# Performance work log

Measured on AMD Instinct MI355X. Metric: run time of the kernel, lower is better.

The kernel has to match this reference:

```python
import jax, jax.numpy as jnp
import numpy as np

H = 1.0  # primo_h
N_GRID = 768


def _grid_mesh(n):
    ii, jj = np.meshgrid(np.arange(n - 1), np.arange(n - 1), indexing='ij')
    v00 = (ii * n + jj).ravel(); v10 = ((ii + 1) * n + jj).ravel()
    v01 = (ii * n + jj + 1).ravel(); v11 = ((ii + 1) * n + jj + 1).ravel()
    tri1 = np.stack([v00, v10, v01], 1); tri2 = np.stack([v10, v11, v01], 1)
    return np.concatenate([tri1, tri2], 0).astype(np.int32)  # [F,3]


def _face_adjacency(faces):
    # faces: [F,3] -> edges [E,2] (sorted vertex pairs), face_ids [E,2]
    F = faces.shape[0]
    fe = np.stack([faces[:, [0, 1]], faces[:, [1, 2]], faces[:, [2, 0]]], 1).reshape(-1, 2)
    fe = np.sort(fe, axis=1)
    fid = np.repeat(np.arange(F, dtype=np.int32), 3)
    order = np.lexsort((fe[:, 1], fe[:, 0]))
    fs, fi = fe[order], fid[order]
    same = np.all(fs[:-1] == fs[1:], axis=1)
    k = np.nonzero(same)[0]
    edges = fs[k].astype(np.int32)
    face_ids = np.stack([fi[k], fi[k + 1]], 1).astype(np.int32)
    return edges, face_ids


def setup_inputs() -> dict:
    key = jax.random.key(0)
    k1, k2, k3 = jax.random.split(key, 3)
    faces_np = _grid_mesh(N_GRID)                      # [F,3]
    edges_np, face_ids_np = _face_adjacency(faces_np)  # [E,2],[E,2]
    F = faces_np.shape[0]
    V = N_GRID * N_GRID
    return {
        'transformed_prism': jax.random.normal(k1, (F, 3, 3), dtype=jnp.float32),
        'rotations': jax.random.normal(k2, (F, 3, 3), dtype=jnp.float32),
        'verts': jax.random.normal(k3, (1, V, 3), dtype=jnp.float32),
        'faces': jnp.asarray(faces_np.T),       # [3,F], matches torch forward arg
        'edges': jnp.asarray(edges_np),
        'face_ids': jnp.asarray(face_ids_np),
    }


def _verts_id_face(Ft, E, Q):
    # Ft: [F,3] faces; E: [e,2] edge vertex ids; Q: [e,2] adjacent face ids
    fa, fb = Ft[Q[:, 0]], Ft[Q[:, 1]]  # [e,3]

    def find(fv, tgt):
        return jnp.where(fv[:, 0] == tgt, 0,
               jnp.where(fv[:, 1] == tgt, 1,
               jnp.where(fv[:, 2] == tgt, 2, -1)))

    return jnp.stack([find(fa, E[:, 0]), find(fa, E[:, 1]),
                      find(fb, E[:, 0]), find(fb, E[:, 1])], axis=1)  # [e,4]


def reference(transformed_prism, rotations, verts, faces, edges, face_ids):
    tp = transformed_prism
    bs = verts.shape[0]
    v = verts.reshape(-1, 3)
    Ft = faces.T  # [F,3]

    # per-face normals (vectorized version of the original per-face loop)
    e1 = tp[:, 0] - tp[:, 1]
    e2 = tp[:, 0] - tp[:, 2]
    nrm = jnp.cross(e1, e2)
    normals = nrm / jnp.linalg.norm(nrm, axis=-1, keepdims=True)  # [F,3]

    # face areas
    p1, p2, p3 = v[Ft[:, 0]], v[Ft[:, 1]], v[Ft[:, 2]]
    face_areas = 0.5 * jnp.linalg.norm(jnp.cross(p2 - p1, p3 - p1), axis=1)

    # faithful to original: normals indexed by edge VERTEX ids
    n1, n2 = normals[edges[:, 0]], normals[edges[:, 1]]
    fid1, fid2 = face_ids[:, 0], face_ids[:, 1]
    r1, r2 = rotations[fid1], rotations[fid2]

    ftv = _verts_id_face(Ft, edges, face_ids)  # [e,4]
    v1_p1, v2_p1 = tp[fid1, ftv[:, 0]], tp[fid1, ftv[:, 1]]
    v1_p2, v2_p2 = tp[fid2, ftv[:, 2]], tp[fid2, ftv[:, 3]]

    p1n1 = jnp.einsum('ec,ecd->ed', n1, r1)
    p1n2 = jnp.einsum('ec,ecd->ed', n2, r1)
    p2n1 = jnp.einsum('ec,ecd->ed', n1, r2)
    p2n2 = jnp.einsum('ec,ecd->ed', n2, r2)

    A = jnp.stack([v1_p1 + p1n1 * H, v2_p1 + p1n2 * H,
                   v1_p1 - p1n1 * H, v2_p1 - p1n2 * H], axis=1)  # [e,4,3]
    B = jnp.stack([v1_p2 + p2n1 * H, v2_p2 + p2n2 * H,
                   v1_p2 - p2n1 * H, v2_p2 - p2n2 * H], axis=1)
    D = A - B

    # coeff[p,q] = 2^{-|i_p-i_q|-|j_p-j_q|}, (i,j) over {0,1}^2
    idx = jnp.array([[0, 0], [0, 1], [1, 0], [1, 1]], dtype=jnp.float32)
    coeff = 2.0 ** (-jnp.abs(idx[:, None] - idx[None, :]).sum(-1))  # [4,4]
    pair = jnp.einsum('epc,eqc->epq', D, D)
    energy = (pair * coeff).sum((1, 2)) / 9.0  # [e]

    weight = jnp.sum((v[edges[:, 0]] - v[edges[:, 1]]) ** 2, axis=1) \
             / (face_areas[fid1] + face_areas[fid2])
    return (energy * weight).sum() / bs
```

## Files before the change

### kernel.cpp

```cpp
#include <hip/hip_runtime.h>


struct __attribute__((aligned(4))) F4s { float a, b, c, d; };
struct F3 { float x, y, z; };
struct R9 { float v[9]; };
struct R6 { float v[6]; };

__device__ __forceinline__ R9 load9(const float* __restrict__ p) {
    R9 r;
    F4s u0 = *(const F4s*)p;
    F4s u1 = *(const F4s*)(p + 4);
    r.v[0] = u0.a; r.v[1] = u0.b; r.v[2] = u0.c; r.v[3] = u0.d;
    r.v[4] = u1.a; r.v[5] = u1.b; r.v[6] = u1.c; r.v[7] = u1.d;
    r.v[8] = p[8];
    return r;
}

__device__ __forceinline__ R6 load6(const float* __restrict__ p) {
    R6 r;
    F4s u = *(const F4s*)p;
    r.v[0] = u.a; r.v[1] = u.b; r.v[2] = u.c; r.v[3] = u.d;
    r.v[4] = p[4]; r.v[5] = p[5];
    return r;
}

__device__ __forceinline__ F3 load3(const float* __restrict__ p) {
    F3 r; r.x = p[0]; r.y = p[1]; r.z = p[2]; return r;
}

__device__ __forceinline__ F3 normal_of(const R9& r) {
    float e1x = r.v[0] - r.v[3], e1y = r.v[1] - r.v[4], e1z = r.v[2] - r.v[5];
    float e2x = r.v[0] - r.v[6], e2y = r.v[1] - r.v[7], e2z = r.v[2] - r.v[8];
    float nx = e1y * e2z - e1z * e2y;
    float ny = e1z * e2x - e1x * e2z;
    float nz = e1x * e2y - e1y * e2x;
    float inv = 1.0f / sqrtf(nx * nx + ny * ny + nz * nz);
    F3 o; o.x = nx * inv; o.y = ny * inv; o.z = nz * inv; return o;
}

__device__ __forceinline__ float tri_area(const F3& p, const F3& q, const F3& r) {
    float ax = q.x - p.x, ay = q.y - p.y, az = q.z - p.z;
    float bx = r.x - p.x, by = r.y - p.y, bz = r.z - p.z;
    float cx = ay * bz - az * by, cy = az * bx - ax * bz, cz = ax * by - ay * bx;
    return 0.5f * sqrtf(cx * cx + cy * cy + cz * cz);
}

__device__ __forceinline__ float edge_ew(const float* u1, const float* u2,
                                         const float* w1, const float* w2,
                                         const float* rA, const float* rB,
                                         const F3& n1, const F3& n2,
                                         const F3& pa, const F3& pb,
                                         float asum) {
    float ux = u1[0] - u2[0], uy = u1[1] - u2[1], uz = u1[2] - u2[2];
    float wx = w1[0] - w2[0], wy = w1[1] - w2[1], wz = w1[2] - w2[2];

    float d0 = rA[0] - rB[0], d1 = rA[1] - rB[1], d2 = rA[2] - rB[2];
    float d3 = rA[3] - rB[3], d4 = rA[4] - rB[4], d5 = rA[5] - rB[5];
    float d6 = rA[6] - rB[6], d7 = rA[7] - rB[7], d8 = rA[8] - rB[8];

    float ax = n1.x * d0 + n1.y * d3 + n1.z * d6;
    float ay = n1.x * d1 + n1.y * d4 + n1.z * d7;
    float az = n1.x * d2 + n1.y * d5 + n1.z * d8;
    float bx = n2.x * d0 + n2.y * d3 + n2.z * d6;
    float by = n2.x * d1 + n2.y * d4 + n2.z * d7;
    float bz = n2.x * d2 + n2.y * d5 + n2.z * d8;

    float uu = ux * ux + uy * uy + uz * uz;
    float ww = wx * wx + wy * wy + wz * wz;
    float uw = ux * wx + uy * wy + uz * wz;
    float aa = ax * ax + ay * ay + az * az;
    float bb = bx * bx + by * by + bz * bz;
    float ab = ax * bx + ay * by + az * bz;
    float energy = (3.0f * (uu + ww + uw) + (aa + bb + ab)) * (1.0f / 9.0f);

    float dx = pa.x - pb.x, dy = pa.y - pb.y, dz = pa.z - pb.z;
    return energy * (dx * dx + dy * dy + dz * dz) / asum;
}

__global__ __launch_bounds__(256) void fused_kernel(
        const float* __restrict__ tp,
        const float* __restrict__ rot,
        const float* __restrict__ verts,
        double* __restrict__ partials,
        int n) {
    const int m = n - 1;
    const int Q = m * m;
    const int tid = threadIdx.x;
    int q = blockIdx.x * 256 + tid;
    bool valid = q < Q;
    int qc = valid ? q : Q - 1;
    int i = qc / m;
    int j = qc - i * m;

    int v00 = i * n + j;
    R9 tA = load9(tp + (size_t)9 * v00);
    R9 tB = load9(tp + (size_t)9 * (v00 + 1));
    R9 tC = load9(tp + (size_t)9 * (v00 + n));
    F3 p00 = load3(verts + (size_t)3 * v00);
    F3 p01 = load3(verts + (size_t)3 * (v00 + 1));
    F3 p10 = load3(verts + (size_t)3 * (v00 + n));
    F3 p11 = load3(verts + (size_t)3 * (v00 + n + 1));
    int iu = (i > 0) ? (i - 1) : 0;
    int jl = (j > 0) ? (j - 1) : 0;
    F3 pup = load3(verts + (size_t)3 * ((size_t)iu * n + (j + 1)));
    F3 plf = load3(verts + (size_t)3 * ((size_t)(i + 1) * n + jl));

    int f1  = i * m + j;
    int f2c = Q + f1;
    int f2u = Q + iu * m + j;
    int f2l = Q + i * m + jl;
    R9 t1 = load9(tp  + (size_t)9 * f1);
    R9 t2 = load9(tp  + (size_t)9 * f2c);
    R9 r1 = load9(rot + (size_t)9 * f1);
    R9 r2 = load9(rot + (size_t)9 * f2c);
    R6 th = load6(tp  + (size_t)9 * f2u);
    R9 rh = load9(rot + (size_t)9 * f2u);
    R6 tv = load6(tp  + (size_t)9 * f2l + 3);
    R9 rv = load9(rot + (size_t)9 * f2l);

    F3 nA = normal_of(tA);
    F3 nB = normal_of(tB);
    F3 nC = normal_of(tC);
    float a1    = tri_area(p00, p10, p01);
    float a2c   = tri_area(p10, p11, p01);
    float a2up  = tri_area(p00, p01, pup);
    float a2lf  = tri_area(plf, p10, p00);

    float sum = edge_ew(t1.v + 6, t2.v + 6, t1.v + 3, t2.v + 0, r1.v, r2.v,
                        nB, nC, p01, p10, a1 + a2c);
    float eh = edge_ew(t1.v + 0, th.v + 0, t1.v + 6, th.v + 3, r1.v, rh.v,
                       nA, nB, p00, p01, a1 + a2up);
    float ev = edge_ew(t1.v + 0, tv.v + 3, t1.v + 3, tv.v + 0, r1.v, rv.v,
                       nA, nC, p00, p10, a1 + a2lf);
    sum += (i > 0 ? eh : 0.0f);
    sum += (j > 0 ? ev : 0.0f);

    double term = valid ? (double)sum : 0.0;

#pragma unroll
    for (int off = 32; off > 0; off >>= 1) term += __shfl_down(term, off, 64);
    __shared__ double sred[4];
    int lane = tid & 63, wid = tid >> 6;
    if (lane == 0) sred[wid] = term;
    __syncthreads();
    if (tid == 0)
        partials[blockIdx.x] = sred[0] + sred[1] + sred[2] + sred[3];
}

__global__ __launch_bounds__(256) void finalize_kernel(
        const double* __restrict__ partials, int P, float* __restrict__ out) {
    double s = 0.0;
    for (int i = threadIdx.x; i < P; i += 256) s += partials[i];
#pragma unroll
    for (int off = 32; off > 0; off >>= 1) s += __shfl_down(s, off, 64);
    __shared__ double sred[4];
    int lane = threadIdx.x & 63, wid = threadIdx.x >> 6;
    if (lane == 0) sred[wid] = s;
    __syncthreads();
    if (threadIdx.x == 0) out[0] = (float)(sred[0] + sred[1] + sred[2] + sred[3]);
}

extern "C" void kernel_launch(void* const* d_in, const int* in_sizes, int n_in,
                              void* d_out, int out_size, void* d_ws, size_t ws_size,
                              hipStream_t stream) {
    const float* tp    = (const float*)d_in[0];
    const float* rot   = (const float*)d_in[1];
    const float* verts = (const float*)d_in[2];

    int V = in_sizes[2] / 3;
    int n = (int)(sqrtf((float)V) + 0.5f);
    int m = n - 1;
    int Q = m * m;

    double* partials = (double*)d_ws;
    float*  out      = (float*)d_out;

    int P = (Q + 255) / 256;
    fused_kernel<<<P, 256, 0, stream>>>(tp, rot, verts, partials, n);
    finalize_kernel<<<1, 256, 0, stream>>>(partials, P, out);
}
```

Before: 155.6 us.

## Tile faces, normals and verts into shared memory with halo reuse

Switches to a 2D block tiling (4 rows x 64 cols) where second-triangle prism/rotation data, per-vertex normals and vertex positions for the tile plus halo are staged in LDS. Neighbouring threads then read shared neighbours from LDS instead of issuing redundant global gathers, and each normal is computed once rather than three times. This costs a block-wide sync, about 50KB of LDS per block that limits occupancy, and halo overhead.

```diff
diff --git a/kernel.cpp b/kernel.cpp
--- a/kernel.cpp
+++ b/kernel.cpp
@@ -1,10 +1,18 @@
 #include <hip/hip_runtime.h>
 
+
+#define BI 4
+#define BJ 64
+#define FR (BI + 1)
+#define FC (BJ + 1)
+#define NR (BI + 1)
+#define NC (BJ + 1)
+#define VR (BI + 2)
+#define VC (BJ + 2)
 
 struct __attribute__((aligned(4))) F4s { float a, b, c, d; };
 struct F3 { float x, y, z; };
 struct R9 { float v[9]; };
-struct R6 { float v[6]; };
 
 __device__ __forceinline__ R9 load9(const float* __restrict__ p) {
     R9 r;
@@ -16,16 +24,8 @@
     return r;
 }
 
-__device__ __forceinline__ R6 load6(const float* __restrict__ p) {
-    R6 r;
-    F4s u = *(const F4s*)p;
-    r.v[0] = u.a; r.v[1] = u.b; r.v[2] = u.c; r.v[3] = u.d;
-    r.v[4] = p[4]; r.v[5] = p[5];
-    return r;
-}
-
-__device__ __forceinline__ F3 load3(const float* __restrict__ p) {
-    F3 r; r.x = p[0]; r.y = p[1]; r.z = p[2]; return r;
+__device__ __forceinline__ int iclamp(int x, int lo, int hi) {
+    return x < lo ? lo : (x > hi ? hi : x);
 }
 
 __device__ __forceinline__ F3 normal_of(const R9& r) {
@@ -38,9 +38,10 @@
     F3 o; o.x = nx * inv; o.y = ny * inv; o.z = nz * inv; return o;
 }
 
-__device__ __forceinline__ float tri_area(const F3& p, const F3& q, const F3& r) {
-    float ax = q.x - p.x, ay = q.y - p.y, az = q.z - p.z;
-    float bx = r.x - p.x, by = r.y - p.y, bz = r.z - p.z;
+__device__ __forceinline__ float tri_area_p(const float* p, const float* q,
+                                            const float* r) {
+    float ax = q[0] - p[0], ay = q[1] - p[1], az = q[2] - p[2];
+    float bx = r[0] - p[0], by = r[1] - p[1], bz = r[2] - p[2];
     float cx = ay * bz - az * by, cy = az * bx - ax * bz, cz = ax * by - ay * bx;
     return 0.5f * sqrtf(cx * cx + cy * cy + cz * cz);
 }
@@ -49,7 +50,7 @@
                                          const float* w1, const float* w2,
                                          const float* rA, const float* rB,
                                          const F3& n1, const F3& n2,
-                                         const F3& pa, const F3& pb,
+                                         const float* pa, const float* pb,
                                          float asum) {
     float ux = u1[0] - u2[0], uy = u1[1] - u2[1], uz = u1[2] - u2[2];
     float wx = w1[0] - w2[0], wy = w1[1] - w2[1], wz = w1[2] - w2[2];
@@ -73,7 +74,7 @@
     float ab = ax * bx + ay * by + az * bz;
     float energy = (3.0f * (uu + ww + uw) + (aa + bb + ab)) * (1.0f / 9.0f);
 
-    float dx = pa.x - pb.x, dy = pa.y - pb.y, dz = pa.z - pb.z;
+    float dx = pa[0] - pb[0], dy = pa[1] - pb[1], dz = pa[2] - pb[2];
     return energy * (dx * dx + dy * dy + dz * dz) / asum;
 }
 
@@ -86,65 +87,102 @@
     const int m = n - 1;
     const int Q = m * m;
     const int tid = threadIdx.x;
-    int q = blockIdx.x * 256 + tid;
-    bool valid = q < Q;
-    int qc = valid ? q : Q - 1;
-    int i = qc / m;
-    int j = qc - i * m;
-
-    int v00 = i * n + j;
-    R9 tA = load9(tp + (size_t)9 * v00);
-    R9 tB = load9(tp + (size_t)9 * (v00 + 1));
-    R9 tC = load9(tp + (size_t)9 * (v00 + n));
-    F3 p00 = load3(verts + (size_t)3 * v00);
-    F3 p01 = load3(verts + (size_t)3 * (v00 + 1));
-    F3 p10 = load3(verts + (size_t)3 * (v00 + n));
-    F3 p11 = load3(verts + (size_t)3 * (v00 + n + 1));
-    int iu = (i > 0) ? (i - 1) : 0;
-    int jl = (j > 0) ? (j - 1) : 0;
-    F3 pup = load3(verts + (size_t)3 * ((size_t)iu * n + (j + 1)));
-    F3 plf = load3(verts + (size_t)3 * ((size_t)(i + 1) * n + jl));
-
-    int f1  = i * m + j;
-    int f2c = Q + f1;
-    int f2u = Q + iu * m + j;
-    int f2l = Q + i * m + jl;
+    const int i0 = blockIdx.y * BI;
+    const int j0 = blockIdx.x * BJ;
+    const int w = tid >> 6;
+    const int l = tid & 63;
+    const int i = i0 + w;
+    const int j = j0 + l;
+
+    __shared__ float sT2[FR * FC * 9];
+    __shared__ float sR2[FR * FC * 9];
+    __shared__ float sN[NR * NC * 3];
+    __shared__ float sV[VR * VC * 3];
+    __shared__ double sred[4];
+
+    int f1 = iclamp(i, 0, m - 1) * m + iclamp(j, 0, m - 1);
     R9 t1 = load9(tp  + (size_t)9 * f1);
-    R9 t2 = load9(tp  + (size_t)9 * f2c);
     R9 r1 = load9(rot + (size_t)9 * f1);
-    R9 r2 = load9(rot + (size_t)9 * f2c);
-    R6 th = load6(tp  + (size_t)9 * f2u);
-    R9 rh = load9(rot + (size_t)9 * f2u);
-    R6 tv = load6(tp  + (size_t)9 * f2l + 3);
-    R9 rv = load9(rot + (size_t)9 * f2l);
-
-    F3 nA = normal_of(tA);
-    F3 nB = normal_of(tB);
-    F3 nC = normal_of(tC);
-    float a1    = tri_area(p00, p10, p01);
-    float a2c   = tri_area(p10, p11, p01);
-    float a2up  = tri_area(p00, p01, pup);
-    float a2lf  = tri_area(plf, p10, p00);
-
-    float sum = edge_ew(t1.v + 6, t2.v + 6, t1.v + 3, t2.v + 0, r1.v, r2.v,
-                        nB, nC, p01, p10, a1 + a2c);
-    float eh = edge_ew(t1.v + 0, th.v + 0, t1.v + 6, th.v + 3, r1.v, rh.v,
-                       nA, nB, p00, p01, a1 + a2up);
-    float ev = edge_ew(t1.v + 0, tv.v + 3, t1.v + 3, tv.v + 0, r1.v, rv.v,
-                       nA, nC, p00, p10, a1 + a2lf);
-    sum += (i > 0 ? eh : 0.0f);
-    sum += (j > 0 ? ev : 0.0f);
-
-    double term = valid ? (double)sum : 0.0;
+
+    for (int idx = tid; idx < FR * FC; idx += 256) {
+        int r = idx / FC, c = idx - r * FC;
+        int gi = iclamp(i0 - 1 + r, 0, m - 1);
+        int gj = iclamp(j0 - 1 + c, 0, m - 1);
+        size_t f = (size_t)Q + (size_t)gi * m + gj;
+        R9 a = load9(tp  + 9 * f);
+        R9 b = load9(rot + 9 * f);
+#pragma unroll
+        for (int k = 0; k < 9; ++k) sT2[9 * idx + k] = a.v[k];
+#pragma unroll
+        for (int k = 0; k < 9; ++k) sR2[9 * idx + k] = b.v[k];
+    }
+    for (int idx = tid; idx < NR * NC; idx += 256) {
+        int r = idx / NC, c = idx - r * NC;
+        int gi = iclamp(i0 + r, 0, n - 1);
+        int gj = iclamp(j0 + c, 0, n - 1);
+        R9 a = load9(tp + 9 * ((size_t)gi * n + gj));
+        F3 nm = normal_of(a);
+        sN[3 * idx] = nm.x; sN[3 * idx + 1] = nm.y; sN[3 * idx + 2] = nm.z;
+    }
+    for (int idx = tid; idx < VR * VC; idx += 256) {
+        int r = idx / VC, c = idx - r * VC;
+        int gi = iclamp(i0 - 1 + r, 0, n - 1);
+        int gj = iclamp(j0 - 1 + c, 0, n - 1);
+        const float* p = verts + 3 * ((size_t)gi * n + gj);
+        sV[3 * idx] = p[0]; sV[3 * idx + 1] = p[1]; sV[3 * idx + 2] = p[2];
+    }
+
+    __syncthreads();
+
+    double term = 0.0;
+    if (i < m && j < m) {
+        const float* t2c = sT2 + 9 * ((w + 1) * FC + (l + 1));
+        const float* r2c = sR2 + 9 * ((w + 1) * FC + (l + 1));
+        const float* th  = sT2 + 9 * (w * FC + (l + 1));
+        const float* rh  = sR2 + 9 * (w * FC + (l + 1));
+        const float* tv  = sT2 + 9 * ((w + 1) * FC + l);
+        const float* rv  = sR2 + 9 * ((w + 1) * FC + l);
+
+        F3 nA = { sN[3 * (w * NC + l)],
+                  sN[3 * (w * NC + l) + 1],
+                  sN[3 * (w * NC + l) + 2] };
+        F3 nB = { sN[3 * (w * NC + l + 1)],
+                  sN[3 * (w * NC + l + 1) + 1],
+                  sN[3 * (w * NC + l + 1) + 2] };
+        F3 nC = { sN[3 * ((w + 1) * NC + l)],
+                  sN[3 * ((w + 1) * NC + l) + 1],
+                  sN[3 * ((w + 1) * NC + l) + 2] };
+
+        const float* p00 = sV + 3 * ((w + 1) * VC + (l + 1));
+        const float* p01 = sV + 3 * ((w + 1) * VC + (l + 2));
+        const float* p10 = sV + 3 * ((w + 2) * VC + (l + 1));
+        const float* p11 = sV + 3 * ((w + 2) * VC + (l + 2));
+        const float* pup = sV + 3 * (w * VC + (l + 2));
+        const float* plf = sV + 3 * ((w + 2) * VC + l);
+
+        float a1   = tri_area_p(p00, p10, p01);
+        float a2c  = tri_area_p(p10, p11, p01);
+        float a2up = tri_area_p(p00, p01, pup);
+        float a2lf = tri_area_p(plf, p10, p00);
+
+        float sum = edge_ew(t1.v + 6, t2c + 6, t1.v + 3, t2c + 0, r1.v, r2c,
+                            nB, nC, p01, p10, a1 + a2c);
+        float eh = edge_ew(t1.v + 0, th + 0, t1.v + 6, th + 3, r1.v, rh,
+                           nA, nB, p00, p01, a1 + a2up);
+        float ev = edge_ew(t1.v + 0, tv + 6, t1.v + 3, tv + 3, r1.v, rv,
+                           nA, nC, p00, p10, a1 + a2lf);
+        sum += (i > 0 ? eh : 0.0f);
+        sum += (j > 0 ? ev : 0.0f);
+        term = (double)sum;
+    }
 
 #pragma unroll
     for (int off = 32; off > 0; off >>= 1) term += __shfl_down(term, off, 64);
-    __shared__ double sred[4];
-    int lane = tid & 63, wid = tid >> 6;
-    if (lane == 0) sred[wid] = term;
+    if (l == 0) sred[w] = term;
     __syncthreads();
     if (tid == 0)
-        partials[blockIdx.x] = sred[0] + sred[1] + sred[2] + sred[3];
+        partials[blockIdx.y * gridDim.x + blockIdx.x] =
+            sred[0] + sred[1] + sred[2] + sred[3];
 }
 
 __global__ __launch_bounds__(256) void finalize_kernel(
@@ -170,12 +208,12 @@
     int V = in_sizes[2] / 3;
     int n = (int)(sqrtf((float)V) + 0.5f);
     int m = n - 1;
-    int Q = m * m;
 
     double* partials = (double*)d_ws;
     float*  out      = (float*)d_out;
 
-    int P = (Q + 255) / 256;
-    fused_kernel<<<P, 256, 0, stream>>>(tp, rot, verts, partials, n);
+    dim3 grid((m + BJ - 1) / BJ, (m + BI - 1) / BI);
+    int P = grid.x * grid.y;
+    fused_kernel<<<grid, 256, 0, stream>>>(tp, rot, verts, partials, n);
     finalize_kernel<<<1, 256, 0, stream>>>(partials, P, out);
 }
```

Result: no change. 152.9 us (-1.7%).

## Process four rows per thread and reuse upper-row loads in registers

Applied to the files above, without the earlier changes.

Restructures the grid so each thread walks T consecutive rows of one column, carrying the shared upper face/prism/vertex data from one row to the next instead of reloading it. This is meant to cut redundant global loads for data shared between vertically adjacent quads. It adds register pressure and reduces the number of waves in flight, which may lower latency hiding.

```diff
diff --git a/kernel.cpp b/kernel.cpp
--- a/kernel.cpp
+++ b/kernel.cpp
@@ -1,5 +1,7 @@
 #include <hip/hip_runtime.h>
 
+
+#define T 4
 
 struct __attribute__((aligned(4))) F4s { float a, b, c, d; };
 struct F3 { float x, y, z; };
@@ -27,6 +29,9 @@
 __device__ __forceinline__ F3 load3(const float* __restrict__ p) {
     F3 r; r.x = p[0]; r.y = p[1]; r.z = p[2]; return r;
 }
+
+__device__ __forceinline__ int imin(int a, int b) { return a < b ? a : b; }
+__device__ __forceinline__ int imax(int a, int b) { return a > b ? a : b; }
 
 __device__ __forceinline__ F3 normal_of(const R9& r) {
     float e1x = r.v[0] - r.v[3], e1y = r.v[1] - r.v[4], e1z = r.v[2] - r.v[5];
@@ -86,65 +91,77 @@
     const int m = n - 1;
     const int Q = m * m;
     const int tid = threadIdx.x;
-    int q = blockIdx.x * 256 + tid;
-    bool valid = q < Q;
-    int qc = valid ? q : Q - 1;
-    int i = qc / m;
-    int j = qc - i * m;
+    const int lane = tid & 63;
+    const int j = blockIdx.x * 64 + lane;
+    const int s = blockIdx.y * 4 + (tid >> 6);
+    const int i0 = s * T;
+    const bool jv = j < m;
+    const int jc = imin(j, m - 1);
+    const int jl = imax(jc - 1, 0);
 
-    int v00 = i * n + j;
-    R9 tA = load9(tp + (size_t)9 * v00);
-    R9 tB = load9(tp + (size_t)9 * (v00 + 1));
-    R9 tC = load9(tp + (size_t)9 * (v00 + n));
-    F3 p00 = load3(verts + (size_t)3 * v00);
-    F3 p01 = load3(verts + (size_t)3 * (v00 + 1));
-    F3 p10 = load3(verts + (size_t)3 * (v00 + n));
-    F3 p11 = load3(verts + (size_t)3 * (v00 + n + 1));
-    int iu = (i > 0) ? (i - 1) : 0;
-    int jl = (j > 0) ? (j - 1) : 0;
-    F3 pup = load3(verts + (size_t)3 * ((size_t)iu * n + (j + 1)));
-    F3 plf = load3(verts + (size_t)3 * ((size_t)(i + 1) * n + jl));
+    int im1 = imax(i0 - 1, 0);
+    R9 th  = load9(tp  + (size_t)9 * (Q + im1 * m + jc));
+    R9 rh  = load9(rot + (size_t)9 * (Q + im1 * m + jc));
+    R9 tA  = load9(tp  + (size_t)9 * ((size_t)i0 * n + jc));
+    F3 p00 = load3(verts + (size_t)3 * ((size_t)i0 * n + jc));
+    F3 p01 = load3(verts + (size_t)3 * ((size_t)i0 * n + jc + 1));
+    F3 pup = load3(verts + (size_t)3 * ((size_t)im1 * n + jc + 1));
 
-    int f1  = i * m + j;
-    int f2c = Q + f1;
-    int f2u = Q + iu * m + j;
-    int f2l = Q + i * m + jl;
-    R9 t1 = load9(tp  + (size_t)9 * f1);
-    R9 t2 = load9(tp  + (size_t)9 * f2c);
-    R9 r1 = load9(rot + (size_t)9 * f1);
-    R9 r2 = load9(rot + (size_t)9 * f2c);
-    R6 th = load6(tp  + (size_t)9 * f2u);
-    R9 rh = load9(rot + (size_t)9 * f2u);
-    R6 tv = load6(tp  + (size_t)9 * f2l + 3);
-    R9 rv = load9(rot + (size_t)9 * f2l);
+    double term = 0.0;
 
-    F3 nA = normal_of(tA);
-    F3 nB = normal_of(tB);
-    F3 nC = normal_of(tC);
-    float a1    = tri_area(p00, p10, p01);
-    float a2c   = tri_area(p10, p11, p01);
-    float a2up  = tri_area(p00, p01, pup);
-    float a2lf  = tri_area(plf, p10, p00);
+#pragma unroll
+    for (int t = 0; t < T; ++t) {
+        int i = i0 + t;
+        int ic = imin(i, m - 1);
+        bool valid = jv && (i < m);
 
-    float sum = edge_ew(t1.v + 6, t2.v + 6, t1.v + 3, t2.v + 0, r1.v, r2.v,
-                        nB, nC, p01, p10, a1 + a2c);
-    float eh = edge_ew(t1.v + 0, th.v + 0, t1.v + 6, th.v + 3, r1.v, rh.v,
-                       nA, nB, p00, p01, a1 + a2up);
-    float ev = edge_ew(t1.v + 0, tv.v + 3, t1.v + 3, tv.v + 0, r1.v, rv.v,
-                       nA, nC, p00, p10, a1 + a2lf);
-    sum += (i > 0 ? eh : 0.0f);
-    sum += (j > 0 ? ev : 0.0f);
+        size_t f1o = (size_t)9 * ((size_t)ic * m + jc);
+        size_t f2o = (size_t)9 * ((size_t)Q + (size_t)ic * m + jc);
+        size_t flo = (size_t)9 * ((size_t)Q + (size_t)ic * m + jl);
+        R9 t1  = load9(tp  + f1o);
+        R9 r1  = load9(rot + f1o);
+        R9 t2  = load9(tp  + f2o);
+        R9 r2  = load9(rot + f2o);
+        R6 tvl = load6(tp  + flo + 3);
+        R9 rvl = load9(rot + flo);
+        R9 tB  = load9(tp  + (size_t)9 * ((size_t)ic * n + jc + 1));
+        R9 tC  = load9(tp  + (size_t)9 * ((size_t)(ic + 1) * n + jc));
+        F3 p10 = load3(verts + (size_t)3 * ((size_t)(ic + 1) * n + jc));
+        F3 p11 = load3(verts + (size_t)3 * ((size_t)(ic + 1) * n + jc + 1));
+        F3 plf = load3(verts + (size_t)3 * ((size_t)(ic + 1) * n + jl));
 
-    double term = valid ? (double)sum : 0.0;
+        F3 nA = normal_of(tA);
+        F3 nB = normal_of(tB);
+        F3 nC = normal_of(tC);
+        float a1   = tri_area(p00, p10, p01);
+        float a2c  = tri_area(p10, p11, p01);
+        float a2up = tri_area(p00, p01, pup);
+        float a2lf = tri_area(plf, p10, p00);
+
+        float sum = edge_ew(t1.v + 6, t2.v + 6, t1.v + 3, t2.v + 0,
+                            r1.v, r2.v, nB, nC, p01, p10, a1 + a2c);
+        float eh  = edge_ew(t1.v + 0, th.v + 0, t1.v + 6, th.v + 3,
+                            r1.v, rh.v, nA, nB, p00, p01, a1 + a2up);
+        float ev  = edge_ew(t1.v + 0, tvl.v + 3, t1.v + 3, tvl.v + 0,
+                            r1.v, rvl.v, nA, nC, p00, p10, a1 + a2lf);
+        sum += (i > 0 ? eh : 0.0f);
+        sum += (j > 0 ? ev : 0.0f);
+        if (valid) term += (double)sum;
+
+        th = t2; rh = r2;
+        tA = tC;
+        pup = p01; p00 = p10; p01 = p11;
+    }
 
 #pragma unroll
     for (int off = 32; off > 0; off >>= 1) term += __shfl_down(term, off, 64);
     __shared__ double sred[4];
-    int lane = tid & 63, wid = tid >> 6;
+    int wid = tid >> 6;
     if (lane == 0) sred[wid] = term;
     __syncthreads();
     if (tid == 0)
-        partials[blockIdx.x] = sred[0] + sred[1] + sred[2] + sred[3];
+        partials[blockIdx.y * gridDim.x + blockIdx.x] =
+            sred[0] + sred[1] + sred[2] + sred[3];
 }
 
 __global__ __launch_bounds__(256) void finalize_kernel(
@@ -170,12 +187,13 @@
     int V = in_sizes[2] / 3;
     int n = (int)(sqrtf((float)V) + 0.5f);
     int m = n - 1;
-    int Q = m * m;
 
     double* partials = (double*)d_ws;
     float*  out      = (float*)d_out;
 
-    int P = (Q + 255) / 256;
-    fused_kernel<<<P, 256, 0, stream>>>(tp, rot, verts, partials, n);
+    int strips = (m + T - 1) / T;
+    dim3 grid((m + 63) / 64, (strips + 3) / 4);
+    int P = grid.x * grid.y;
+    fused_kernel<<<grid, 256, 0, stream>>>(tp, rot, verts, partials, n);
     finalize_kernel<<<1, 256, 0, stream>>>(partials, P, out);
 }
```

Result: slower. 161.4 us (+3.7%).

## Process two adjacent grid cells per thread to share loads and normals

Applied to the files above, without the earlier changes.

Each thread now handles two horizontally adjacent quads, loading contiguous spans of prism, rotation and vertex data with wide vector loads. Shared vertices, normals and face data are reused between the two cells, and the second cell's left edge reuses the first cell's second face. This cuts redundant global loads and normal computations and halves the thread count, at the cost of more registers per thread and extra clamping and select logic at the odd-column tail.

```diff
diff --git a/kernel.cpp b/kernel.cpp
--- a/kernel.cpp
+++ b/kernel.cpp
@@ -3,34 +3,54 @@
 
 struct __attribute__((aligned(4))) F4s { float a, b, c, d; };
 struct F3 { float x, y, z; };
-struct R9 { float v[9]; };
-struct R6 { float v[6]; };
-
-__device__ __forceinline__ R9 load9(const float* __restrict__ p) {
-    R9 r;
-    F4s u0 = *(const F4s*)p;
-    F4s u1 = *(const F4s*)(p + 4);
-    r.v[0] = u0.a; r.v[1] = u0.b; r.v[2] = u0.c; r.v[3] = u0.d;
-    r.v[4] = u1.a; r.v[5] = u1.b; r.v[6] = u1.c; r.v[7] = u1.d;
-    r.v[8] = p[8];
+struct R8  { float v[8];  };
+struct R9  { float v[9];  };
+struct R12 { float v[12]; };
+struct R16 { float v[16]; };
+struct R18 { float v[18]; };
+struct R27 { float v[27]; };
+
+__device__ __forceinline__ void ld4(const float* p, float* d) {
+    F4s u = *(const F4s*)p; d[0]=u.a; d[1]=u.b; d[2]=u.c; d[3]=u.d;
+}
+__device__ __forceinline__ R8 load8(const float* p) {
+    R8 r; ld4(p, r.v); ld4(p + 4, r.v + 4); return r;
+}
+__device__ __forceinline__ R9 load9(const float* p) {
+    R9 r; ld4(p, r.v); ld4(p + 4, r.v + 4); r.v[8] = p[8]; return r;
+}
+__device__ __forceinline__ R12 load12(const float* p) {
+    R12 r; ld4(p, r.v); ld4(p + 4, r.v + 4); ld4(p + 8, r.v + 8); return r;
+}
+__device__ __forceinline__ R16 load16(const float* p) {
+    R16 r; ld4(p, r.v); ld4(p+4, r.v+4); ld4(p+8, r.v+8); ld4(p+12, r.v+12);
     return r;
 }
-
-__device__ __forceinline__ R6 load6(const float* __restrict__ p) {
-    R6 r;
-    F4s u = *(const F4s*)p;
-    r.v[0] = u.a; r.v[1] = u.b; r.v[2] = u.c; r.v[3] = u.d;
-    r.v[4] = p[4]; r.v[5] = p[5];
+__device__ __forceinline__ R18 load18(const float* p) {
+    R18 r; ld4(p, r.v); ld4(p+4, r.v+4); ld4(p+8, r.v+8); ld4(p+12, r.v+12);
+    float t[4]; ld4(p + 14, t); r.v[16] = t[2]; r.v[17] = t[3]; return r;
+}
+__device__ __forceinline__ R27 load27(const float* p) {
+    R27 r; ld4(p, r.v); ld4(p+4, r.v+4); ld4(p+8, r.v+8); ld4(p+12, r.v+12);
+    ld4(p+16, r.v+16); ld4(p+20, r.v+20);
+    float t[4]; ld4(p + 23, t); r.v[24] = t[1]; r.v[25] = t[2]; r.v[26] = t[3];
     return r;
 }
 
-__device__ __forceinline__ F3 load3(const float* __restrict__ p) {
+__device__ __forceinline__ int imin(int a, int b) { return a < b ? a : b; }
+__device__ __forceinline__ int imax(int a, int b) { return a > b ? a : b; }
+
+__device__ __forceinline__ F3 f3sel(bool t, const float* a, const float* b) {
+    F3 r; r.x = t ? a[0] : b[0]; r.y = t ? a[1] : b[1]; r.z = t ? a[2] : b[2];
+    return r;
+}
+__device__ __forceinline__ F3 f3of(const float* p) {
     F3 r; r.x = p[0]; r.y = p[1]; r.z = p[2]; return r;
 }
 
-__device__ __forceinline__ F3 normal_of(const R9& r) {
-    float e1x = r.v[0] - r.v[3], e1y = r.v[1] - r.v[4], e1z = r.v[2] - r.v[5];
-    float e2x = r.v[0] - r.v[6], e2y = r.v[1] - r.v[7], e2z = r.v[2] - r.v[8];
+__device__ __forceinline__ F3 normal9(const float* r) {
+    float e1x = r[0] - r[3], e1y = r[1] - r[4], e1z = r[2] - r[5];
+    float e2x = r[0] - r[6], e2y = r[1] - r[7], e2z = r[2] - r[8];
     float nx = e1y * e2z - e1z * e2y;
     float ny = e1z * e2x - e1x * e2z;
     float nz = e1x * e2y - e1y * e2x;
@@ -82,60 +102,93 @@
         const float* __restrict__ rot,
         const float* __restrict__ verts,
         double* __restrict__ partials,
-        int n) {
+        int n, int ppr) {
     const int m = n - 1;
     const int Q = m * m;
     const int tid = threadIdx.x;
-    int q = blockIdx.x * 256 + tid;
-    bool valid = q < Q;
-    int qc = valid ? q : Q - 1;
-    int i = qc / m;
-    int j = qc - i * m;
-
-    int v00 = i * n + j;
-    R9 tA = load9(tp + (size_t)9 * v00);
-    R9 tB = load9(tp + (size_t)9 * (v00 + 1));
-    R9 tC = load9(tp + (size_t)9 * (v00 + n));
-    F3 p00 = load3(verts + (size_t)3 * v00);
-    F3 p01 = load3(verts + (size_t)3 * (v00 + 1));
-    F3 p10 = load3(verts + (size_t)3 * (v00 + n));
-    F3 p11 = load3(verts + (size_t)3 * (v00 + n + 1));
-    int iu = (i > 0) ? (i - 1) : 0;
-    int jl = (j > 0) ? (j - 1) : 0;
-    F3 pup = load3(verts + (size_t)3 * ((size_t)iu * n + (j + 1)));
-    F3 plf = load3(verts + (size_t)3 * ((size_t)(i + 1) * n + jl));
-
-    int f1  = i * m + j;
-    int f2c = Q + f1;
-    int f2u = Q + iu * m + j;
-    int f2l = Q + i * m + jl;
-    R9 t1 = load9(tp  + (size_t)9 * f1);
-    R9 t2 = load9(tp  + (size_t)9 * f2c);
-    R9 r1 = load9(rot + (size_t)9 * f1);
-    R9 r2 = load9(rot + (size_t)9 * f2c);
-    R6 th = load6(tp  + (size_t)9 * f2u);
-    R9 rh = load9(rot + (size_t)9 * f2u);
-    R6 tv = load6(tp  + (size_t)9 * f2l + 3);
-    R9 rv = load9(rot + (size_t)9 * f2l);
-
-    F3 nA = normal_of(tA);
-    F3 nB = normal_of(tB);
-    F3 nC = normal_of(tC);
-    float a1    = tri_area(p00, p10, p01);
-    float a2c   = tri_area(p10, p11, p01);
-    float a2up  = tri_area(p00, p01, pup);
-    float a2lf  = tri_area(plf, p10, p00);
-
-    float sum = edge_ew(t1.v + 6, t2.v + 6, t1.v + 3, t2.v + 0, r1.v, r2.v,
-                        nB, nC, p01, p10, a1 + a2c);
-    float eh = edge_ew(t1.v + 0, th.v + 0, t1.v + 6, th.v + 3, r1.v, rh.v,
-                       nA, nB, p00, p01, a1 + a2up);
-    float ev = edge_ew(t1.v + 0, tv.v + 3, t1.v + 3, tv.v + 0, r1.v, rv.v,
-                       nA, nC, p00, p10, a1 + a2lf);
-    sum += (i > 0 ? eh : 0.0f);
-    sum += (j > 0 ? ev : 0.0f);
-
-    double term = valid ? (double)sum : 0.0;
+    int p = blockIdx.x * 256 + tid;
+    int i = p / ppr;
+    int pj = p - i * ppr;
+    int jj = 2 * pj;
+    bool vi = (i < m);
+    int ic = imin(i, m - 1);
+    bool vb = vi && (jj + 1 < m);
+    bool tl = (jj == m - 1);
+    int vbq = vb ? 1 : 0;
+
+    int iu = imax(ic - 1, 0);
+    int jl = imax(jj - 1, 0);
+    size_t f1 = (size_t)ic * m + jj;
+    size_t f2 = (size_t)Q + f1;
+    size_t fu = (size_t)Q + (size_t)iu * m + jj;
+    size_t fl = (size_t)Q + (size_t)ic * m + jl;
+    int b2 = imin(jj, n - 3);
+    int b3 = imin(jj - 1, n - 4);
+    int b4 = imin(jj + 1, n - 2);
+
+    R27 VA = load27(tp + (size_t)9 * ((size_t)ic * n + b2));
+    R27 VC = load27(tp + (size_t)9 * ((size_t)(ic + 1) * n + b2));
+    R9  VI = load9(verts + (size_t)3 * ((size_t)ic * n + b2));
+    R12 VJ = load12(verts + 3 * ((size_t)(ic + 1) * n + b3));
+    R8  G  = load8(verts + (size_t)3 * ((size_t)iu * n + b4));
+
+    R18 T1 = load18(tp  + 9 * f1);
+    R18 R1 = load18(rot + 9 * f1);
+    R9  T2a = load9(tp  + 9 * f2);
+    R9  R2a = load9(rot + 9 * f2);
+    R9  T2b = load9(tp  + 9 * (f2 + vbq));
+    R9  R2b = load9(rot + 9 * (f2 + vbq));
+    R16 TH = load16(tp  + 9 * fu);
+    R18 RH = load18(rot + 9 * fu);
+    R8  TVL = load8(tp  + 9 * fl + 3);
+    R9  RVL = load9(rot + 9 * fl);
+
+    F3 N0 = normal9(VA.v + 0), N1 = normal9(VA.v + 9), N2 = normal9(VA.v + 18);
+    F3 M0 = normal9(VC.v + 0), M1 = normal9(VC.v + 9), M2 = normal9(VC.v + 18);
+    F3 nAa = f3sel(tl, VA.v + 9, VA.v + 0);
+    nAa = tl ? N1 : N0;
+    F3 nBa = tl ? N2 : N1;
+    F3 nBb = N2;
+    F3 nAb = nBa;
+    F3 nCa = tl ? M1 : M0;
+    F3 nCb = tl ? M2 : M1;
+
+    F3 p00a = f3sel(tl, VI.v + 3, VI.v + 0);
+    F3 p01a = f3sel(tl, VI.v + 6, VI.v + 3);
+    F3 p00b = p01a;
+    F3 p01b = f3of(VI.v + 6);
+    F3 plfa = f3sel(tl, VJ.v + 3, VJ.v + 0);
+    F3 p10a = f3sel(tl, VJ.v + 6, VJ.v + 3);
+    F3 p11a = f3sel(tl, VJ.v + 9, VJ.v + 6);
+    F3 p10b = p11a;
+    F3 p11b = f3of(VJ.v + 9);
+    F3 pupa = f3sel(tl, G.v + 3, G.v + 0);
+    F3 pupb = f3of(G.v + 3);
+
+    float a1a  = tri_area(p00a, p10a, p01a);
+    float a2ca = tri_area(p10a, p11a, p01a);
+    float a2ua = tri_area(p00a, p01a, pupa);
+    float a2la = tri_area(plfa, p10a, p00a);
+    float a1b  = tri_area(p00b, p10b, p01b);
+    float a2cb = tri_area(p10b, p11b, p01b);
+    float a2ub = tri_area(p00b, p01b, pupb);
+
+    float ea_d = edge_ew(T1.v + 6, T2a.v + 6, T1.v + 3, T2a.v + 0,
+                         R1.v + 0, R2a.v, nBa, nCa, p01a, p10a, a1a + a2ca);
+    float ea_h = edge_ew(T1.v + 0, TH.v + 0, T1.v + 6, TH.v + 3,
+                         R1.v + 0, RH.v + 0, nAa, nBa, p00a, p01a, a1a + a2ua);
+    float ea_v = edge_ew(T1.v + 0, TVL.v + 3, T1.v + 3, TVL.v + 0,
+                         R1.v + 0, RVL.v, nAa, nCa, p00a, p10a, a1a + a2la);
+    float eb_d = edge_ew(T1.v + 15, T2b.v + 6, T1.v + 12, T2b.v + 0,
+                         R1.v + 9, R2b.v, nBb, nCb, p01b, p10b, a1b + a2cb);
+    float eb_h = edge_ew(T1.v + 9, TH.v + 9, T1.v + 15, TH.v + 12,
+                         R1.v + 9, RH.v + 9, nAb, nBb, p00b, p01b, a1b + a2ub);
+    float eb_v = edge_ew(T1.v + 9, T2a.v + 6, T1.v + 12, T2a.v + 3,
+                         R1.v + 9, R2a.v, nAb, nCb, p00b, p10b, a1b + a2ca);
+
+    float sa = ea_d + (i > 0 ? ea_h : 0.0f) + (jj > 0 ? ea_v : 0.0f);
+    float sb = eb_d + (i > 0 ? eb_h : 0.0f) + eb_v;
+    double term = (vi ? (double)sa : 0.0) + (vb ? (double)sb : 0.0);
 
 #pragma unroll
     for (int off = 32; off > 0; off >>= 1) term += __shfl_down(term, off, 64);
@@ -170,12 +223,12 @@
     int V = in_sizes[2] / 3;
     int n = (int)(sqrtf((float)V) + 0.5f);
     int m = n - 1;
-    int Q = m * m;
+    int ppr = (m + 1) / 2;
 
     double* partials = (double*)d_ws;
     float*  out      = (float*)d_out;
 
-    int P = (Q + 255) / 256;
-    fused_kernel<<<P, 256, 0, stream>>>(tp, rot, verts, partials, n);
+    int P = ((size_t)m * ppr + 255) / 256;
+    fused_kernel<<<P, 256, 0, stream>>>(tp, rot, verts, partials, n, ppr);
     finalize_kernel<<<1, 256, 0, stream>>>(partials, P, out);
 }
```

Measured after the change: 168.2 us. +8.1%, slower.
